# Optimization experiments

Measured on AMD Instinct MI355X. Metric: run time of the kernel, lower is better.

Reference implementation:

```python
import jax, jax.numpy as jnp
import numpy as np

B, NI, H, NC = 524288, 32, 128, 64


def _masks(ni, h):
    deg_in = jnp.arange(ni)                     # input layer: arange % ni == arange
    deg_hid = jnp.arange(h) % (ni - 1)
    deg_out = jnp.arange(2 * ni) % ni - 1
    m1 = (deg_hid[:, None] >= deg_in[None, :]).astype(jnp.float32)   # [H, NI]
    m2 = (deg_hid[:, None] >= deg_hid[None, :]).astype(jnp.float32)  # [H, H]
    m3 = (deg_out[:, None] >= deg_hid[None, :]).astype(jnp.float32)  # [2NI, H]
    return m1, m2, m3


def setup_inputs() -> dict:
    key = jax.random.key(0)
    ks = jax.random.split(key, 9)
    s = 0.05
    return {
        "x": jax.random.normal(ks[0], (B, NI), jnp.float32),
        "cond": jax.random.normal(ks[1], (B, NC), jnp.float32),
        "W1": jax.random.normal(ks[2], (H, NI), jnp.float32) * s,
        "b1": jnp.zeros((H,), jnp.float32),
        "Wc": jax.random.normal(ks[3], (H, NC), jnp.float32) * s,
        "W2": jax.random.normal(ks[4], (H, H), jnp.float32) * s,
        "b2": jnp.zeros((H,), jnp.float32),
        "W3": jax.random.normal(ks[5], (2 * NI, H), jnp.float32) * s,
        "b3": jnp.zeros((2 * NI,), jnp.float32),
    }


def reference(x, cond, W1, b1, Wc, W2, b2, W3, b3):
    ni = x.shape[1]
    h_dim = W1.shape[0]
    m1, m2, m3 = _masks(ni, h_dim)
    # joiner: masked linear + conditioning linear (no bias on cond)
    h = x @ (W1 * m1).T + b1 + cond @ Wc.T            # [B, H]
    h = jax.nn.relu(h)
    h = jax.nn.relu(h @ (W2 * m2).T + b2)             # [B, H]
    o = h @ (W3 * m3).T + b3                          # [B, 2NI]
    m_, a = o[:, :ni], o[:, ni:]
    a = jnp.clip(a, -5.0, 5.0)
    u = (x - m_) * jnp.exp(-a)
    logdet = -jnp.sum(a, axis=-1, keepdims=True)
    return u, logdet
```

## Files before the change

### kernel.cpp

```cpp
#include <hip/hip_runtime.h>


#define B_ROWS 524288
#define NI 32
#define HD 128
#define NC 64

#define L2_BASE 48
#define L3_BASE 112
#define N_FRAGS 144

typedef _Float16 half4 __attribute__((ext_vector_type(4)));
typedef float f32x4 __attribute__((ext_vector_type(4)));

__device__ inline half4 cvt4(f32x4 v) {
  half4 h;
  h[0] = (_Float16)v[0]; h[1] = (_Float16)v[1];
  h[2] = (_Float16)v[2]; h[3] = (_Float16)v[3];
  return h;
}

__global__ void prep_weights(const float* __restrict__ W1, const float* __restrict__ Wc,
                             const float* __restrict__ W2, const float* __restrict__ W3,
                             _Float16* __restrict__ wf) {
  int tid = blockIdx.x * blockDim.x + threadIdx.x;
  if (tid >= N_FRAGS * 64) return;
  int frag = tid >> 6;
  int lane = tid & 63;
  int q = lane >> 4, c = lane & 15;
  int L, jt, kt;
  if (frag < L2_BASE)      { L = 0; jt = frag / 6;             kt = frag % 6; }
  else if (frag < L3_BASE) { L = 1; jt = (frag - L2_BASE) >> 3; kt = (frag - L2_BASE) & 7; }
  else                     { L = 2; jt = (frag - L3_BASE) >> 3; kt = (frag - L3_BASE) & 7; }
  int j = jt * 16 + c;
  half4 v;
#pragma unroll
  for (int i = 0; i < 4; ++i) {
    int k = kt * 16 + q * 4 + i;
    float w;
    if (L == 0) {
      if (k < NI) w = ((j % 31) >= k) ? W1[j * NI + k] : 0.f;
      else        w = Wc[j * NC + (k - NI)];
    } else if (L == 1) {
      w = ((j % 31) >= (k % 31)) ? W2[j * HD + k] : 0.f;
    } else {
      w = (((j % 32) - 1) >= (k % 31)) ? W3[j * HD + k] : 0.f;
    }
    v[i] = (_Float16)w;
  }
  *(half4*)(wf + (size_t)tid * 4) = v;
}

__global__ __launch_bounds__(256, 3) void made_fused(
    const float* __restrict__ x, const float* __restrict__ cond,
    const float* __restrict__ b1, const float* __restrict__ b2,
    const float* __restrict__ b3, const _Float16* __restrict__ wf,
    float* __restrict__ out) {
  __shared__ _Float16 wlds[96 * 256];

  const int tid  = threadIdx.x;
  const int lane = tid & 63;
  const int wid  = tid >> 6;
  const int q = lane >> 4, c = lane & 15;
  const long rowbase = ((long)blockIdx.x * 4 + wid) * 32;

  {
    const f32x4* src = (const f32x4*)(wf + L2_BASE * 256);
    f32x4* dst = (f32x4*)wlds;
#pragma unroll
    for (int k = 0; k < 12; ++k) dst[tid + k * 256] = src[tid + k * 256];
  }

  half4 bf[6][2];
#pragma unroll
  for (int nt = 0; nt < 2; ++nt) {
    const float* xr = x    + (rowbase + nt * 16 + c) * NI;
    const float* cr = cond + (rowbase + nt * 16 + c) * NC;
    bf[0][nt] = cvt4(*(const f32x4*)(xr + q * 4));
    bf[1][nt] = cvt4(*(const f32x4*)(xr + 16 + q * 4));
    bf[2][nt] = cvt4(*(const f32x4*)(cr + q * 4));
    bf[3][nt] = cvt4(*(const f32x4*)(cr + 16 + q * 4));
    bf[4][nt] = cvt4(*(const f32x4*)(cr + 32 + q * 4));
    bf[5][nt] = cvt4(*(const f32x4*)(cr + 48 + q * 4));
  }

  f32x4 acc[8][2];
#pragma unroll
  for (int jt = 0; jt < 8; ++jt) {
    f32x4 bv = *(const f32x4*)(b1 + jt * 16 + q * 4);
#pragma unroll
    for (int nt = 0; nt < 2; ++nt) acc[jt][nt] = bv;
  }
#pragma unroll
  for (int jt = 0; jt < 8; ++jt) {
#pragma unroll
    for (int kt = 0; kt < 6; ++kt) {
      half4 a = *(const half4*)(wf + (((jt * 6 + kt) * 64 + lane) << 2));
#pragma unroll
      for (int nt = 0; nt < 2; ++nt)
        acc[jt][nt] = __builtin_amdgcn_mfma_f32_16x16x16f16(a, bf[kt][nt], acc[jt][nt], 0, 0, 0);
    }
  }
  half4 h1[8][2];
#pragma unroll
  for (int jt = 0; jt < 8; ++jt)
#pragma unroll
    for (int nt = 0; nt < 2; ++nt) {
      f32x4 v = acc[jt][nt];
      v[0] = fmaxf(v[0], 0.f); v[1] = fmaxf(v[1], 0.f);
      v[2] = fmaxf(v[2], 0.f); v[3] = fmaxf(v[3], 0.f);
      h1[jt][nt] = cvt4(v);
    }

  __syncthreads();

#pragma unroll
  for (int jt = 0; jt < 8; ++jt) {
    f32x4 bv = *(const f32x4*)(b2 + jt * 16 + q * 4);
#pragma unroll
    for (int nt = 0; nt < 2; ++nt) acc[jt][nt] = bv;
  }
#pragma unroll
  for (int jt = 0; jt < 8; ++jt) {
#pragma unroll
    for (int kt = 0; kt < 8; ++kt) {
      half4 a = *(const half4*)(wlds + (((jt * 8 + kt) * 64 + lane) << 2));
#pragma unroll
      for (int nt = 0; nt < 2; ++nt)
        acc[jt][nt] = __builtin_amdgcn_mfma_f32_16x16x16f16(a, h1[kt][nt], acc[jt][nt], 0, 0, 0);
    }
  }
  half4 h2[8][2];
#pragma unroll
  for (int jt = 0; jt < 8; ++jt)
#pragma unroll
    for (int nt = 0; nt < 2; ++nt) {
      f32x4 v = acc[jt][nt];
      v[0] = fmaxf(v[0], 0.f); v[1] = fmaxf(v[1], 0.f);
      v[2] = fmaxf(v[2], 0.f); v[3] = fmaxf(v[3], 0.f);
      h2[jt][nt] = cvt4(v);
    }

  f32x4 acc3[4][2];
#pragma unroll
  for (int jt = 0; jt < 4; ++jt) {
    f32x4 bv = *(const f32x4*)(b3 + jt * 16 + q * 4);
#pragma unroll
    for (int nt = 0; nt < 2; ++nt) acc3[jt][nt] = bv;
  }
#pragma unroll
  for (int jt = 0; jt < 4; ++jt) {
#pragma unroll
    for (int kt = 0; kt < 8; ++kt) {
      half4 a = *(const half4*)(wlds + (((64 + jt * 8 + kt) * 64 + lane) << 2));
#pragma unroll
      for (int nt = 0; nt < 2; ++nt)
        acc3[jt][nt] = __builtin_amdgcn_mfma_f32_16x16x16f16(a, h2[kt][nt], acc3[jt][nt], 0, 0, 0);
    }
  }

#pragma unroll
  for (int nt = 0; nt < 2; ++nt) {
    long m = rowbase + nt * 16 + c;
    const float* xr = x + m * NI;
    f32x4 xa = *(const f32x4*)(xr + q * 4);
    f32x4 xb = *(const f32x4*)(xr + 16 + q * 4);
    f32x4 mva = acc3[0][nt], mvb = acc3[1][nt];
    f32x4 ava = acc3[2][nt], avb = acc3[3][nt];
    f32x4 ua, ub;
    float s = 0.f;
#pragma unroll
    for (int i = 0; i < 4; ++i) {
      float aa = fminf(fmaxf(ava[i], -5.f), 5.f);
      float ab = fminf(fmaxf(avb[i], -5.f), 5.f);
      ua[i] = (xa[i] - mva[i]) * __expf(-aa);
      ub[i] = (xb[i] - mvb[i]) * __expf(-ab);
      s += aa + ab;
    }
    *(f32x4*)(out + m * NI + q * 4) = ua;
    *(f32x4*)(out + m * NI + 16 + q * 4) = ub;
    s += __shfl_xor(s, 16);
    s += __shfl_xor(s, 32);
    if (q == 0) out[(long)B_ROWS * NI + m] = -s;
  }
}

extern "C" void kernel_launch(void* const* d_in, const int* in_sizes, int n_in,
                              void* d_out, int out_size, void* d_ws, size_t ws_size,
                              hipStream_t stream) {
  const float* x    = (const float*)d_in[0];
  const float* cond = (const float*)d_in[1];
  const float* W1   = (const float*)d_in[2];
  const float* b1   = (const float*)d_in[3];
  const float* Wc   = (const float*)d_in[4];
  const float* W2   = (const float*)d_in[5];
  const float* b2   = (const float*)d_in[6];
  const float* W3   = (const float*)d_in[7];
  const float* b3   = (const float*)d_in[8];
  _Float16* wf = (_Float16*)d_ws;

  prep_weights<<<(N_FRAGS * 64 + 255) / 256, 256, 0, stream>>>(W1, Wc, W2, W3, wf);
  made_fused<<<B_ROWS / 128, 256, 0, stream>>>(x, cond, b1, b2, b3, wf, (float*)d_out);
}
```

Before: 306.0 us.

## Switch to 16x16x32 f16 MFMA, 512-thread blocks, and direct global-to-LDS weight loads

Repacks the weight fragments into half8 layout for the 16x16x32 MFMA, which halves the MFMA instruction count and the number of fragment loads. Blocks double to 512 threads so each block's LDS weight copy is amortized over more rows. The staging copy now uses global_load_lds to move weights straight into LDS without going through registers. Accumulators are processed in halves to reduce register pressure toward 4 blocks per CU. Risks include relying on the intrinsic completing before the barrier and having fewer blocks in flight overall.

```diff
diff --git a/kernel.cpp b/kernel.cpp
--- a/kernel.cpp
+++ b/kernel.cpp
@@ -6,17 +6,25 @@
 #define HD 128
 #define NC 64
 
-#define L2_BASE 48
-#define L3_BASE 112
-#define N_FRAGS 144
-
-typedef _Float16 half4 __attribute__((ext_vector_type(4)));
+#define L2_BASE 24
+#define L3_BASE 56
+#define N_FRAGS 72
+
+typedef _Float16 half8 __attribute__((ext_vector_type(8)));
 typedef float f32x4 __attribute__((ext_vector_type(4)));
 
-__device__ inline half4 cvt4(f32x4 v) {
-  half4 h;
-  h[0] = (_Float16)v[0]; h[1] = (_Float16)v[1];
-  h[2] = (_Float16)v[2]; h[3] = (_Float16)v[3];
+__device__ inline f32x4 relu4(f32x4 v) {
+  v[0] = fmaxf(v[0], 0.f); v[1] = fmaxf(v[1], 0.f);
+  v[2] = fmaxf(v[2], 0.f); v[3] = fmaxf(v[3], 0.f);
+  return v;
+}
+
+__device__ inline half8 cvt8(f32x4 lo, f32x4 hi) {
+  half8 h;
+  h[0] = (_Float16)lo[0]; h[1] = (_Float16)lo[1];
+  h[2] = (_Float16)lo[2]; h[3] = (_Float16)lo[3];
+  h[4] = (_Float16)hi[0]; h[5] = (_Float16)hi[1];
+  h[6] = (_Float16)hi[2]; h[7] = (_Float16)hi[3];
   return h;
 }
 
@@ -29,14 +37,14 @@
   int lane = tid & 63;
   int q = lane >> 4, c = lane & 15;
   int L, jt, kt;
-  if (frag < L2_BASE)      { L = 0; jt = frag / 6;             kt = frag % 6; }
-  else if (frag < L3_BASE) { L = 1; jt = (frag - L2_BASE) >> 3; kt = (frag - L2_BASE) & 7; }
-  else                     { L = 2; jt = (frag - L3_BASE) >> 3; kt = (frag - L3_BASE) & 7; }
+  if (frag < L2_BASE)      { L = 0; jt = frag / 3;              kt = frag % 3; }
+  else if (frag < L3_BASE) { L = 1; jt = (frag - L2_BASE) >> 2; kt = (frag - L2_BASE) & 3; }
+  else                     { L = 2; jt = (frag - L3_BASE) >> 2; kt = (frag - L3_BASE) & 3; }
   int j = jt * 16 + c;
-  half4 v;
-#pragma unroll
-  for (int i = 0; i < 4; ++i) {
-    int k = kt * 16 + q * 4 + i;
+  half8 v;
+#pragma unroll
+  for (int e = 0; e < 8; ++e) {
+    int k = kt * 32 + (e >> 2) * 16 + q * 4 + (e & 3);
     float w;
     if (L == 0) {
       if (k < NI) w = ((j % 31) >= k) ? W1[j * NI + k] : 0.f;
@@ -46,118 +54,115 @@
     } else {
       w = (((j % 32) - 1) >= (k % 31)) ? W3[j * HD + k] : 0.f;
     }
-    v[i] = (_Float16)w;
-  }
-  *(half4*)(wf + (size_t)tid * 4) = v;
-}
-
-__global__ __launch_bounds__(256, 3) void made_fused(
+    v[e] = (_Float16)w;
+  }
+  *(half8*)(wf + (size_t)tid * 8) = v;
+}
+
+__global__ __launch_bounds__(512, 4) void made_fused(
     const float* __restrict__ x, const float* __restrict__ cond,
     const float* __restrict__ b1, const float* __restrict__ b2,
     const float* __restrict__ b3, const _Float16* __restrict__ wf,
     float* __restrict__ out) {
-  __shared__ _Float16 wlds[96 * 256];
+  __shared__ __align__(16) _Float16 wlds[48 * 512];
 
   const int tid  = threadIdx.x;
   const int lane = tid & 63;
   const int wid  = tid >> 6;
   const int q = lane >> 4, c = lane & 15;
-  const long rowbase = ((long)blockIdx.x * 4 + wid) * 32;
+  const long rowbase = ((long)blockIdx.x * 8 + wid) * 32;
 
   {
-    const f32x4* src = (const f32x4*)(wf + L2_BASE * 256);
-    f32x4* dst = (f32x4*)wlds;
-#pragma unroll
-    for (int k = 0; k < 12; ++k) dst[tid + k * 256] = src[tid + k * 256];
-  }
-
-  half4 bf[6][2];
+    const char* gsrc = (const char*)(wf + L2_BASE * 512) + wid * 6144;
+    char* lbase = (char*)wlds + wid * 6144;
+#pragma unroll
+    for (int i = 0; i < 6; ++i) {
+      __builtin_amdgcn_global_load_lds(
+          (const __attribute__((address_space(1))) void*)(gsrc + i * 1024 + lane * 16),
+          (__attribute__((address_space(3))) void*)(lbase + i * 1024),
+          16, 0, 0);
+    }
+  }
+
+  half8 bf[3][2];
 #pragma unroll
   for (int nt = 0; nt < 2; ++nt) {
     const float* xr = x    + (rowbase + nt * 16 + c) * NI;
     const float* cr = cond + (rowbase + nt * 16 + c) * NC;
-    bf[0][nt] = cvt4(*(const f32x4*)(xr + q * 4));
-    bf[1][nt] = cvt4(*(const f32x4*)(xr + 16 + q * 4));
-    bf[2][nt] = cvt4(*(const f32x4*)(cr + q * 4));
-    bf[3][nt] = cvt4(*(const f32x4*)(cr + 16 + q * 4));
-    bf[4][nt] = cvt4(*(const f32x4*)(cr + 32 + q * 4));
-    bf[5][nt] = cvt4(*(const f32x4*)(cr + 48 + q * 4));
-  }
-
-  f32x4 acc[8][2];
-#pragma unroll
-  for (int jt = 0; jt < 8; ++jt) {
-    f32x4 bv = *(const f32x4*)(b1 + jt * 16 + q * 4);
-#pragma unroll
-    for (int nt = 0; nt < 2; ++nt) acc[jt][nt] = bv;
-  }
-#pragma unroll
-  for (int jt = 0; jt < 8; ++jt) {
-#pragma unroll
-    for (int kt = 0; kt < 6; ++kt) {
-      half4 a = *(const half4*)(wf + (((jt * 6 + kt) * 64 + lane) << 2));
+    bf[0][nt] = cvt8(*(const f32x4*)(xr + q * 4), *(const f32x4*)(xr + 16 + q * 4));
+    bf[1][nt] = cvt8(*(const f32x4*)(cr + q * 4), *(const f32x4*)(cr + 16 + q * 4));
+    bf[2][nt] = cvt8(*(const f32x4*)(cr + 32 + q * 4), *(const f32x4*)(cr + 48 + q * 4));
+  }
+
+  f32x4 acc[4][2];
+  half8 h1[4][2];
+#pragma unroll
+  for (int jh = 0; jh < 2; ++jh) {
+#pragma unroll
+    for (int j4 = 0; j4 < 4; ++j4) {
+      f32x4 bv = *(const f32x4*)(b1 + (jh * 4 + j4) * 16 + q * 4);
+      acc[j4][0] = bv; acc[j4][1] = bv;
+    }
+#pragma unroll
+    for (int j4 = 0; j4 < 4; ++j4) {
+      int jt = jh * 4 + j4;
+#pragma unroll
+      for (int kt = 0; kt < 3; ++kt) {
+        half8 a = *(const half8*)(wf + (((jt * 3 + kt) * 64 + lane) << 3));
+#pragma unroll
+        for (int nt = 0; nt < 2; ++nt)
+          acc[j4][nt] = __builtin_amdgcn_mfma_f32_16x16x32_f16(a, bf[kt][nt], acc[j4][nt], 0, 0, 0);
+      }
+    }
+#pragma unroll
+    for (int p = 0; p < 2; ++p)
 #pragma unroll
       for (int nt = 0; nt < 2; ++nt)
-        acc[jt][nt] = __builtin_amdgcn_mfma_f32_16x16x16f16(a, bf[kt][nt], acc[jt][nt], 0, 0, 0);
-    }
-  }
-  half4 h1[8][2];
-#pragma unroll
-  for (int jt = 0; jt < 8; ++jt)
-#pragma unroll
-    for (int nt = 0; nt < 2; ++nt) {
-      f32x4 v = acc[jt][nt];
-      v[0] = fmaxf(v[0], 0.f); v[1] = fmaxf(v[1], 0.f);
-      v[2] = fmaxf(v[2], 0.f); v[3] = fmaxf(v[3], 0.f);
-      h1[jt][nt] = cvt4(v);
-    }
+        h1[jh * 2 + p][nt] = cvt8(relu4(acc[p * 2][nt]), relu4(acc[p * 2 + 1][nt]));
+  }
 
   __syncthreads();
 
-#pragma unroll
-  for (int jt = 0; jt < 8; ++jt) {
-    f32x4 bv = *(const f32x4*)(b2 + jt * 16 + q * 4);
-#pragma unroll
-    for (int nt = 0; nt < 2; ++nt) acc[jt][nt] = bv;
-  }
-#pragma unroll
-  for (int jt = 0; jt < 8; ++jt) {
-#pragma unroll
-    for (int kt = 0; kt < 8; ++kt) {
-      half4 a = *(const half4*)(wlds + (((jt * 8 + kt) * 64 + lane) << 2));
+  half8 h2[4][2];
+#pragma unroll
+  for (int jh = 0; jh < 2; ++jh) {
+#pragma unroll
+    for (int j4 = 0; j4 < 4; ++j4) {
+      f32x4 bv = *(const f32x4*)(b2 + (jh * 4 + j4) * 16 + q * 4);
+      acc[j4][0] = bv; acc[j4][1] = bv;
+    }
+#pragma unroll
+    for (int j4 = 0; j4 < 4; ++j4) {
+      int jt = jh * 4 + j4;
+#pragma unroll
+      for (int kt = 0; kt < 4; ++kt) {
+        half8 a = *(const half8*)(wlds + (((jt * 4 + kt) * 64 + lane) << 3));
+#pragma unroll
+        for (int nt = 0; nt < 2; ++nt)
+          acc[j4][nt] = __builtin_amdgcn_mfma_f32_16x16x32_f16(a, h1[kt][nt], acc[j4][nt], 0, 0, 0);
+      }
+    }
+#pragma unroll
+    for (int p = 0; p < 2; ++p)
 #pragma unroll
       for (int nt = 0; nt < 2; ++nt)
-        acc[jt][nt] = __builtin_amdgcn_mfma_f32_16x16x16f16(a, h1[kt][nt], acc[jt][nt], 0, 0, 0);
-    }
-  }
-  half4 h2[8][2];
-#pragma unroll
-  for (int jt = 0; jt < 8; ++jt)
-#pragma unroll
-    for (int nt = 0; nt < 2; ++nt) {
-      f32x4 v = acc[jt][nt];
-      v[0] = fmaxf(v[0], 0.f); v[1] = fmaxf(v[1], 0.f);
-      v[2] = fmaxf(v[2], 0.f); v[3] = fmaxf(v[3], 0.f);
-      h2[jt][nt] = cvt4(v);
-    }
-
-  f32x4 acc3[4][2];
+        h2[jh * 2 + p][nt] = cvt8(relu4(acc[p * 2][nt]), relu4(acc[p * 2 + 1][nt]));
+  }
+
 #pragma unroll
   for (int jt = 0; jt < 4; ++jt) {
     f32x4 bv = *(const f32x4*)(b3 + jt * 16 + q * 4);
-#pragma unroll
-    for (int nt = 0; nt < 2; ++nt) acc3[jt][nt] = bv;
-  }
-#pragma unroll
-  for (int jt = 0; jt < 4; ++jt) {
-#pragma unroll
-    for (int kt = 0; kt < 8; ++kt) {
-      half4 a = *(const half4*)(wlds + (((64 + jt * 8 + kt) * 64 + lane) << 2));
+    acc[jt][0] = bv; acc[jt][1] = bv;
+  }
+#pragma unroll
+  for (int jt = 0; jt < 4; ++jt)
+#pragma unroll
+    for (int kt = 0; kt < 4; ++kt) {
+      half8 a = *(const half8*)(wlds + (((32 + jt * 4 + kt) * 64 + lane) << 3));
 #pragma unroll
       for (int nt = 0; nt < 2; ++nt)
-        acc3[jt][nt] = __builtin_amdgcn_mfma_f32_16x16x16f16(a, h2[kt][nt], acc3[jt][nt], 0, 0, 0);
-    }
-  }
+        acc[jt][nt] = __builtin_amdgcn_mfma_f32_16x16x32_f16(a, h2[kt][nt], acc[jt][nt], 0, 0, 0);
+    }
 
 #pragma unroll
   for (int nt = 0; nt < 2; ++nt) {
@@ -165,8 +170,8 @@
     const float* xr = x + m * NI;
     f32x4 xa = *(const f32x4*)(xr + q * 4);
     f32x4 xb = *(const f32x4*)(xr + 16 + q * 4);
-    f32x4 mva = acc3[0][nt], mvb = acc3[1][nt];
-    f32x4 ava = acc3[2][nt], avb = acc3[3][nt];
+    f32x4 mva = acc[0][nt], mvb = acc[1][nt];
+    f32x4 ava = acc[2][nt], avb = acc[3][nt];
     f32x4 ua, ub;
     float s = 0.f;
 #pragma unroll
@@ -200,5 +205,5 @@
   _Float16* wf = (_Float16*)d_ws;
 
   prep_weights<<<(N_FRAGS * 64 + 255) / 256, 256, 0, stream>>>(W1, Wc, W2, W3, wf);
-  made_fused<<<B_ROWS / 128, 256, 0, stream>>>(x, cond, b1, b2, b3, wf, (float*)d_out);
-}
+  made_fused<<<B_ROWS / 256, 512, 0, stream>>>(x, cond, b1, b2, b3, wf, (float*)d_out);
+}
```

After: 292.9 us. 4.3% less time.
